# Performance work log

Hardware: AMD Instinct MI355X
Metric: run time of the kernel (lower is better)

Reference implementation:

```python
import jax, jax.numpy as jnp
import numpy as np

N = 100000   # num_nodes
D = 128      # input_dim
DO = 128     # output_dim
V = 3        # num_views/relations
E = 500000   # edges per view
C = 2        # num_classes
H = D // 2   # label-attention hidden
VH = DO // 2 # view-attention hidden
EPS = 1e-5


def setup_inputs() -> dict:
    key = jax.random.key(0)
    ks = jax.random.split(key, 20)
    s = 0.05
    def nrm(k, shape):
        return jax.random.normal(k, shape, dtype=jnp.float32) * s
    return {
        'features': jax.random.normal(ks[0], (N, D), dtype=jnp.float32),
        'edge_src': jax.random.randint(ks[1], (V, E), 0, N, dtype=jnp.int32),
        'edge_dst': jax.random.randint(ks[2], (V, E), 0, N, dtype=jnp.int32),
        'edge_w': jax.random.uniform(ks[3], (V, E), dtype=jnp.float32),
        'clsW': nrm(ks[4], (D, C)), 'clsb': jnp.zeros((C,), jnp.float32),
        'attW1': nrm(ks[5], (C, D, H)), 'attb1': jnp.zeros((C, H), jnp.float32),
        'attW2': nrm(ks[6], (C, H)), 'attb2': jnp.zeros((C,), jnp.float32),
        'att_bias': jnp.float32(0.1),
        'relW': nrm(ks[7], (V, D, DO)), 'relb': jnp.zeros((V, DO), jnp.float32),
        'gateW': nrm(ks[8], (V, DO, DO)), 'gateb': jnp.zeros((V, DO), jnp.float32),
        'view_pref': jax.random.normal(ks[9], (V, DO), dtype=jnp.float32),
        'vattW1': nrm(ks[10], (DO, VH)), 'vattb1': jnp.zeros((VH,), jnp.float32),
        'vattW2': nrm(ks[11], (VH,)), 'vattb2': jnp.float32(0.0),
        'selfW': nrm(ks[12], (D, DO)), 'selfb': jnp.zeros((DO,), jnp.float32),
        'featW': nrm(ks[13], (D, DO)), 'featb': jnp.zeros((DO,), jnp.float32),
        'fusW': nrm(ks[14], (2 * DO, DO)), 'fusb': jnp.zeros((DO,), jnp.float32),
        'ln_g': jnp.ones((DO,), jnp.float32), 'ln_b': jnp.zeros((DO,), jnp.float32),
    }


def reference(features, edge_src, edge_dst, edge_w,
              clsW, clsb, attW1, attb1, attW2, attb2, att_bias,
              relW, relb, gateW, gateb,
              view_pref, vattW1, vattb1, vattW2, vattb2,
              selfW, selfb, featW, featb, fusW, fusb, ln_g, ln_b):
    # --- LabelAwareAttention ---
    class_probs = jax.nn.softmax(features @ clsW + clsb, axis=-1)          # [N,C]
    h = jax.nn.relu(jnp.einsum('nd,cdh->cnh', features, attW1) + attb1[:, None, :])
    scores = jax.nn.sigmoid(jnp.einsum('cnh,ch->cn', h, attW2) + attb2[:, None])
    node_att = jnp.sum(scores.T * class_probs, axis=-1) + att_bias         # [N]

    # --- per-view RelationAggregator (num_relations=1 -> relation weight is 1) ---
    src_f = features[edge_src]                                             # [V,E,D]
    msg = (jnp.einsum('ved,vdo->veo', src_f, relW) + relb[:, None, :]) \
          * edge_w[..., None]                                              # [V,E,DO]
    agg = jax.vmap(lambda m, d: jax.ops.segment_sum(m, d, num_segments=N))(
        msg, edge_dst)                                                     # [V,N,DO]
    gate = jax.nn.sigmoid(jnp.einsum('vno,vop->vnp', agg, gateW) + gateb[:, None, :])
    view_out = gate * agg                                                  # [V,N,DO]

    # --- ViewLevelAttention ---
    vh = jax.nn.relu(jnp.einsum('vno,oh->vnh', view_out * view_pref[:, None, :], vattW1) + vattb1)
    vscores = jnp.einsum('vnh,h->vn', vh, vattW2) + vattb2                 # [V,N]
    vweights = jax.nn.softmax(vscores, axis=0)                             # softmax over views
    combined = jnp.sum(view_out * vweights[..., None], axis=0)             # [N,DO]

    # --- fusion + residual + layer norm (dropout=0, eval) ---
    self_out = features @ selfW + selfb
    transformed = features @ featW + featb
    weighted = combined * node_att[:, None]
    fused = jax.nn.relu(jnp.concatenate([self_out, weighted], axis=-1) @ fusW + fusb)
    out = fused + transformed
    mu = jnp.mean(out, axis=-1, keepdims=True)
    var = jnp.var(out, axis=-1, keepdims=True)
    out = (out - mu) / jnp.sqrt(var + EPS) * ln_g + ln_b
    return out, class_probs
```

## Files before the change

### kernel.cpp

```cpp
#include <hip/hip_runtime.h>
#include <hip/hip_bf16.h>

#define NN 100000
#define DD 128
#define VV 3
#define EE 500000
#define TOT (VV * NN)
#define NB ((TOT + 255) / 256)
#define RGB ((NN + 127) / 128)

typedef unsigned short u16;
typedef unsigned int u32;
typedef short s8v __attribute__((ext_vector_type(8)));
typedef float f4v __attribute__((ext_vector_type(4)));

__device__ __forceinline__ float bf2f(u16 u) {
    return __uint_as_float(((u32)u) << 16);
}
__device__ __forceinline__ u16 f2bf(float f) {
    u32 x = __float_as_uint(f);
    u32 r = (x + 0x7fffu + ((x >> 16) & 1u)) >> 16;
    return (u16)r;
}

// ... 86 lines not shown
    #pragma unroll
    for (int rep = 0; rep < 512 / NT; ++rep) {
        int flat = rep * NT + tid;
        int n = flat >> 4;
        int c8 = flat & 15;
        uint4 q = *reinterpret_cast<const uint4*>(src + (size_t)n * 128 + c8 * 8);
        float* d = Xs + n * XSTR + c8 * 8;
        d[0] = bf2f((u16)(q.x & 0xffffu)); d[1] = bf2f((u16)(q.x >> 16));
        d[2] = bf2f((u16)(q.y & 0xffffu)); d[3] = bf2f((u16)(q.y >> 16));
        d[4] = bf2f((u16)(q.z & 0xffffu)); d[5] = bf2f((u16)(q.z >> 16));
        d[6] = bf2f((u16)(q.w & 0xffffu)); d[7] = bf2f((u16)(q.w >> 16));
    }
}


__device__ __forceinline__ void stageWf(u16 (*Wf)[136], const u16* __restrict__ src, int tid) {
    #pragma unroll
    for (int rep = 0; rep < 8; ++rep) {
        int flat = rep * 256 + tid;
        int n = flat >> 4, c8 = flat & 15;
        *reinterpret_cast<uint4*>(&Wf[n][c8 * 8]) =
            *reinterpret_cast<const uint4*>(src + (size_t)n * DD + c8 * 8);
    }
}

__device__ __forceinline__ void stageWtHalf(u16 (*Wt)[72], const u16* __restrict__ src, int tid) {
    #pragma unroll
    for (int rep = 0; rep < 4; ++rep) {
        int flat = rep * 256 + tid;
        int n = flat >> 3, c8 = flat & 7;
        *reinterpret_cast<uint4*>(&Wt[n][c8 * 8]) =
            *reinterpret_cast<const uint4*>(src + (size_t)n * DD + c8 * 8);
    }
}

__device__ __forceinline__ void stageX(u16 (*Wf)[136], const u16* __restrict__ src,
                                       int row0, int tid) {
    #pragma unroll
    for (int rep = 0; rep < 8; ++rep) {
        int flat = rep * 256 + tid;
        int n = flat >> 4, c8 = flat & 15;
        int gr = row0 + n; if (gr >= NN) gr = NN - 1;
        *reinterpret_cast<uint4*>(&Wf[n][c8 * 8]) =
            *reinterpret_cast<const uint4*>(src + (size_t)gr * DD + c8 * 8);
    }
}

__device__ __forceinline__ void loadFrags(s8v af[2][2][2], u16 (*Wf)[136],
                                          int wv, int l15, int quad) {
    #pragma unroll
    for (int h = 0; h < 2; ++h)
        #pragma unroll
        for (int t = 0; t < 2; ++t) {
            int kl = h * 64 + t * 32 + quad * 8;
            af[h][t][0] = *reinterpret_cast<const s8v*>(&Wf[wv * 32 + l15][kl]);
            af[h][t][1] = *reinterpret_cast<const s8v*>(&Wf[wv * 32 + 16 + l15][kl]);
        }
}

__device__ __forceinline__ void mfmaWt8(f4v acc[2][8], const s8v af[2][2][2], int h,
                                        u16 (*Wt)[72], int l15, int quad) {
    #pragma unroll
    for (int t = 0; t < 2; ++t) {
        int kl = t * 32 + quad * 8;
        #pragma unroll
        for (int c = 0; c < 8; ++c) {
            s8v b = *reinterpret_cast<const s8v*>(&Wt[c * 16 + l15][kl]);
            acc[0][c] = __builtin_amdgcn_mfma_f32_16x16x32_bf16(af[h][t][0], b, acc[0][c], 0, 0, 0);
            acc[1][c] = __builtin_amdgcn_mfma_f32_16x16x32_bf16(af[h][t][1], b, acc[1][c], 0, 0, 0);
        }
    }
}

__device__ __forceinline__ void mfmaWfFull(f4v acc[2][8], const s8v af[2][2][2],
                                           u16 (*Wf)[136], int l15, int quad) {
    #pragma unroll
    for (int h = 0; h < 2; ++h)
        #pragma unroll
        for (int t = 0; t < 2; ++t) {
            int kl = h * 64 + t * 32 + quad * 8;
            #pragma unroll
            for (int c = 0; c < 8; ++c) {
                s8v b = *reinterpret_cast<const s8v*>(&Wf[c * 16 + l15][kl]);
                acc[0][c] = __builtin_amdgcn_mfma_f32_16x16x32_bf16(af[h][t][0], b, acc[0][c], 0, 0, 0);
                acc[1][c] = __builtin_amdgcn_mfma_f32_16x16x32_bf16(af[h][t][1], b, acc[1][c], 0, 0, 0);
            }
        }
}

__global__ void prep_kernel(const float* __restrict__ selfW, const float* __restrict__ selfb,
                            const float* __restrict__ fusW, const float* __restrict__ fusb,
                            float* __restrict__ Wsf, float* __restrict__ c1) {
    int o = threadIdx.x;
    int k = blockIdx.x;
    if (k < 128) {
        float acc = 0.f;
        for (int m = 0; m < 128; ++m)
            acc += selfW[k * 128 + m] * fusW[m * 128 + o];
// ... 206 lines not shown
    int src = 0, dst = 0; float w = 0.f;
    if (lane == 0) {
        src = esrc[eg]; dst = edst[eg]; w = ew[eg];
    }
    src = __shfl(src, 0, 32);
    dst = __shfl(dst, 0, 32);
    w   = __shfl(w, 0, 32);
    const float* fr = feat + (size_t)src * DD + lane * 4;
    float4 q = *reinterpret_cast<const float4*>(fr);
    u16* outp = aggB + ((size_t)v * NN + dst) * DD + lane * 4;
    atomAddBf16x2(outp,     w * q.x, w * q.y);
    atomAddBf16x2(outp + 2, w * q.z, w * q.w);
    if (lane == 0) atomicAdd(wsum + v * NN + dst, w);
}

__global__ __launch_bounds__(256) void fused_mfma_kernel(
        const u16* __restrict__ featB, const u16* __restrict__ aggB,
        const u16* __restrict__ attW1B,
        const float* __restrict__ clsW, const float* __restrict__ clsb,
        const float* __restrict__ attb1, const float* __restrict__ attW2,
        const float* __restrict__ attb2, const float* __restrict__ att_bias,
        const u16* __restrict__ relWb, const float* __restrict__ relb,
        const u16* __restrict__ W12b, const float* __restrict__ rgbv,
        const float* __restrict__ gateb,
        const u16* __restrict__ vattW1p, const float* __restrict__ vattb1,
        const float* __restrict__ vattW2, const float* __restrict__ vattb2,
        const float* __restrict__ wsum,
        const u16* __restrict__ WsfB, const u16* __restrict__ featWB,
        const u16* __restrict__ fusWbB,
        const float* __restrict__ c1, const float* __restrict__ featb,
        const float* __restrict__ ln_g, const float* __restrict__ ln_b,
        float* __restrict__ outp, float* __restrict__ probs_out) {
    __shared__ u16 Wf[128][136];
    __shared__ u16 Wt[128][72];
    int tid = threadIdx.x;
    int wv = tid >> 6, lane = tid & 63;
    int quad = lane >> 4, l15 = lane & 15;
    int row0 = blockIdx.x * 128;
    const float L2E = 1.4426950408889634f;

    float na[2][4];
    {
        stageX(Wf, featB, row0, tid);
        stageWtHalf(Wt, attW1B, tid);
        __syncthreads();
        s8v af[2][2][2];
        loadFrags(af, Wf, wv, l15, quad);
        f4v accL[2][8];
        #pragma unroll
        for (int rt = 0; rt < 2; ++rt)
            #pragma unroll
            for (int c = 0; c < 8; ++c)
                accL[rt][c] = f4v{0.f, 0.f, 0.f, 0.f};
        mfmaWt8(accL, af, 0, Wt, l15, quad);
        __syncthreads();
        stageWtHalf(Wt, attW1B + 64, tid);
        __syncthreads();
        mfmaWt8(accL, af, 1, Wt, l15, quad);

        float ab1[8], aw2[8];
        #pragma unroll
        for (int c = 0; c < 8; ++c) {
            int col = c * 16 + l15;
            ab1[c] = attb1[col];
            aw2[c] = attW2[col];
        }
        float cw0[8], cw1[8];
        #pragma unroll
        for (int j = 0; j < 8; ++j) {
            int k = l15 * 8 + j;
            cw0[j] = clsW[k * 2];
            cw1[j] = clsW[k * 2 + 1];
        }
        float cb0 = clsb[0], cb1 = clsb[1];
        float b20 = attb2[0], b21 = attb2[1];
        float abias = att_bias[0];

        #pragma unroll
        for (int rt = 0; rt < 2; ++rt)
            #pragma unroll
            for (int r = 0; r < 4; ++r) {
                int n = wv * 32 + rt * 16 + quad * 4 + r;
                int gr = row0 + n;
                float p0 = 0.f, p1 = 0.f;
                #pragma unroll
                for (int c = 0; c < 4; ++c) {
                    float hv = accL[rt][c][r] + ab1[c];
                    hv = hv > 0.f ? hv : 0.f;
                    p0 += hv * aw2[c];
                }
                #pragma unroll
                for (int c = 4; c < 8; ++c) {
                    float hv = accL[rt][c][r] + ab1[c];
                    hv = hv > 0.f ? hv : 0.f;
                    p1 += hv * aw2[c];
                }
                uint4 q = *reinterpret_cast<const uint4*>(&Wf[n][l15 * 8]);
                float f[8];
                f[0] = bf2f((u16)(q.x & 0xffffu)); f[1] = bf2f((u16)(q.x >> 16));
                f[2] = bf2f((u16)(q.y & 0xffffu)); f[3] = bf2f((u16)(q.y >> 16));
                f[4] = bf2f((u16)(q.z & 0xffffu)); f[5] = bf2f((u16)(q.z >> 16));
                f[6] = bf2f((u16)(q.w & 0xffffu)); f[7] = bf2f((u16)(q.w >> 16));
                float l0 = 0.f, l1 = 0.f;
                #pragma unroll
                for (int j = 0; j < 8; ++j) {
                    l0 = fmaf(f[j], cw0[j], l0);
                    l1 = fmaf(f[j], cw1[j], l1);
                }
                #pragma unroll
                for (int m = 1; m < 16; m <<= 1) {
                    p0 += __shfl_xor(p0, m);
                    p1 += __shfl_xor(p1, m);
                    l0 += __shfl_xor(l0, m);
                    l1 += __shfl_xor(l1, m);
                }
                float s0 = 1.f / (1.f + expf(-(p0 + b20)));
                float s1 = 1.f / (1.f + expf(-(p1 + b21)));
                l0 += cb0; l1 += cb1;
                float mm = fmaxf(l0, l1);
                float e0 = expf(l0 - mm), e1 = expf(l1 - mm);
                float inv = 1.f / (e0 + e1);
                float q0 = e0 * inv, q1 = e1 * inv;
                na[rt][r] = q0 * s0 + q1 * s1 + abias;
                if (l15 == 0 && gr < NN) {
                    probs_out[gr * 2]     = q0;
                    probs_out[gr * 2 + 1] = q1;
                }
            }
    }

    float Cacc[2][8][4];
    float mrun[2][4], Srun[2][4];
    #pragma unroll
    for (int rt = 0; rt < 2; ++rt)
        #pragma unroll
        for (int r = 0; r < 4; ++r) { mrun[rt][r] = -3.0e38f; Srun[rt][r] = 0.f; }
    #pragma unroll
    for (int rt = 0; rt < 2; ++rt)
        #pragma unroll
        for (int c = 0; c < 8; ++c)
            #pragma unroll
            for (int r = 0; r < 4; ++r) Cacc[rt][c][r] = 0.f;

    for (int v = 0; v < VV; ++v) {
        const size_t vbase = (size_t)v * NN;
        __syncthreads();
        stageX(Wf, aggB + vbase * DD, row0, tid);
        __syncthreads();
        s8v af[2][2][2];
        loadFrags(af, Wf, wv, l15, quad);
        __syncthreads();
        const u16* W1 = relWb + (size_t)v * DD * DD;
        const u16* W2 = W12b + (size_t)v * DD * DD;
        stageWf(Wf, W1, tid);
        stageWtHalf(Wt, W2, tid);
        __syncthreads();
        f4v acc2[2][8];
        #pragma unroll
        for (int rt = 0; rt < 2; ++rt)
            #pragma unroll
            for (int c = 0; c < 8; ++c)
                acc2[rt][c] = f4v{0.f, 0.f, 0.f, 0.f};
        mfmaWt8(acc2, af, 0, Wt, l15, quad);
        __syncthreads();
        stageWtHalf(Wt, W2 + 64, tid);
        __syncthreads();
        mfmaWt8(acc2, af, 1, Wt, l15, quad);

        float wsn[2][4];
        #pragma unroll
        for (int rt = 0; rt < 2; ++rt)
            #pragma unroll
            for (int r = 0; r < 4; ++r) {
                int gr = row0 + wv * 32 + rt * 16 + quad * 4 + r;
                wsn[rt][r] = wsum[vbase + (gr < NN ? gr : NN - 1)];
            }
        u32 gpk[2][8][2];
        #pragma unroll
        for (int c = 0; c < 8; ++c) {
            int col = c * 16 + l15;
            float rg2 = rgbv[v * DD + col];
            float gb2 = gateb[v * DD + col];
            #pragma unroll
            for (int rt = 0; rt < 2; ++rt)
                #pragma unroll
                for (int rp = 0; rp < 2; ++rp) {
                    float g0 = fsigmoid(acc2[rt][c][2 * rp]     + wsn[rt][2 * rp] * rg2 + gb2);
                    float g1 = fsigmoid(acc2[rt][c][2 * rp + 1] + wsn[rt][2 * rp + 1] * rg2 + gb2);
                    gpk[rt][c][rp] = (u32)f2bf(g0) | ((u32)f2bf(g1) << 16);
                }
        }
        f4v acc1[2][8];
        #pragma unroll
        for (int rt = 0; rt < 2; ++rt)
            #pragma unroll
            for (int c = 0; c < 8; ++c)
                acc1[rt][c] = f4v{0.f, 0.f, 0.f, 0.f};
        mfmaWfFull(acc1, af, Wf, l15, quad);
        #pragma unroll
        for (int c = 0; c < 8; ++c) {
            float rbc = relb[v * DD + c * 16 + l15];
            #pragma unroll
            for (int rt = 0; rt < 2; ++rt)
                #pragma unroll
                for (int r = 0; r < 4; ++r) {
                    float a = acc1[rt][c][r] + wsn[rt][r] * rbc;
                    u32 gp = gpk[rt][c][r >> 1];
                    float g = bf2f((u16)((r & 1) ? (gp >> 16) : (gp & 0xffffu)));
                    acc1[rt][c][r] = g * a;
                }
        }
        __syncthreads();
        #pragma unroll
        for (int rt = 0; rt < 2; ++rt)
            #pragma unroll
            for (int c = 0; c < 8; ++c)
                #pragma unroll
                for (int r = 0; r < 4; ++r)
                    Wf[wv * 32 + rt * 16 + quad * 4 + r][c * 16 + l15] =
                        f2bf(acc1[rt][c][r]);
        {
            const u16* Wv = vattW1p + (size_t)v * 64 * DD;
            #pragma unroll
            for (int rep = 0; rep < 4; ++rep) {
                int flat = rep * 256 + tid;
                int n = flat >> 4, c8 = flat & 15;
                uint4 q = *reinterpret_cast<const uint4*>(Wv + (size_t)n * DD + c8 * 8);
                int half = c8 >> 3;
                *reinterpret_cast<uint4*>(&Wt[half * 64 + n][(c8 & 7) * 8]) = q;
            }
        }
        __syncthreads();
        s8v a2[2][2][2];
        loadFrags(a2, Wf, wv, l15, quad);
        f4v acc3[2][4];
        #pragma unroll
        for (int rt = 0; rt < 2; ++rt)
            #pragma unroll
            for (int c = 0; c < 4; ++c)
                acc3[rt][c] = f4v{0.f, 0.f, 0.f, 0.f};
        #pragma unroll
        for (int h = 0; h < 2; ++h)
            #pragma unroll
            for (int t = 0; t < 2; ++t) {
                int kl = t * 32 + quad * 8;
                #pragma unroll
                for (int c = 0; c < 4; ++c) {
                    s8v b = *reinterpret_cast<const s8v*>(&Wt[h * 64 + c * 16 + l15][kl]);
                    acc3[0][c] = __builtin_amdgcn_mfma_f32_16x16x32_bf16(a2[h][t][0], b, acc3[0][c], 0, 0, 0);
                    acc3[1][c] = __builtin_amdgcn_mfma_f32_16x16x32_bf16(a2[h][t][1], b, acc3[1][c], 0, 0, 0);
                }
            }
        float vb1[4], vw2[4];
        #pragma unroll
        for (int c = 0; c < 4; ++c) {
            int col = c * 16 + l15;
            vb1[c] = vattb1[col];
            vw2[c] = vattW2[col];
        }
        float vb2 = vattb2[0];
        #pragma unroll
        for (int rt = 0; rt < 2; ++rt)
            #pragma unroll
            for (int r = 0; r < 4; ++r) {
                float p = 0.f;
                #pragma unroll
                for (int c = 0; c < 4; ++c) {
                    float hv = acc3[rt][c][r] + vb1[c];
                    hv = hv > 0.f ? hv : 0.f;
                    p += hv * vw2[c];
                }
                #pragma unroll
                for (int m = 1; m < 16; m <<= 1)
                    p += __shfl_xor(p, m);
                float s = p + vb2;
                float mn = fmaxf(mrun[rt][r], s);
                float sc = fexp2((mrun[rt][r] - mn) * L2E);
                float es = fexp2((s - mn) * L2E);
                Srun[rt][r] = Srun[rt][r] * sc + es;
                mrun[rt][r] = mn;
                #pragma unroll
                for (int c = 0; c < 8; ++c)
                    Cacc[rt][c][r] = Cacc[rt][c][r] * sc + es * acc1[rt][c][r];
            }
    }

    float wrow[2][4];
    #pragma unroll
    for (int rt = 0; rt < 2; ++rt)
        #pragma unroll
        for (int r = 0; r < 4; ++r)
            wrow[rt][r] = na[rt][r] * frcp(Srun[rt][r]);
    __syncthreads();
    #pragma unroll
    for (int rt = 0; rt < 2; ++rt)
        #pragma unroll
        for (int c = 0; c < 8; ++c)
            #pragma unroll
            for (int r = 0; r < 4; ++r)
                Wf[wv * 32 + rt * 16 + quad * 4 + r][c * 16 + l15] =
                    f2bf(Cacc[rt][c][r] * wrow[rt][r]);
    __syncthreads();
    s8v a2[2][2][2];
    loadFrags(a2, Wf, wv, l15, quad);
    __syncthreads();
    stageX(Wf, featB, row0, tid);
    __syncthreads();
    s8v af[2][2][2];
    loadFrags(af, Wf, wv, l15, quad);
    __syncthreads();
    stageWf(Wf, WsfB, tid);
    stageWtHalf(Wt, featWB, tid);
    __syncthreads();
    f4v acc1[2][8], acc2[2][8];
    #pragma unroll
    for (int rt = 0; rt < 2; ++rt)
        #pragma unroll
        for (int c = 0; c < 8; ++c) {
            acc1[rt][c] = f4v{0.f, 0.f, 0.f, 0.f};
            acc2[rt][c] = f4v{0.f, 0.f, 0.f, 0.f};
        }
    mfmaWfFull(acc1, af, Wf, l15, quad);
    mfmaWt8(acc2, af, 0, Wt, l15, quad);
    __syncthreads();
    stageWf(Wf, fusWbB, tid);
    stageWtHalf(Wt, featWB + 64, tid);
    __syncthreads();
    mfmaWt8(acc2, af, 1, Wt, l15, quad);
    mfmaWfFull(acc1, a2, Wf, l15, quad);

    float c1j[8], fbj[8], gj[8], bj[8];
    #pragma unroll
    for (int c = 0; c < 8; ++c) {
        int col = c * 16 + l15;
        c1j[c] = c1[col];
        fbj[c] = featb[col];
        gj[c]  = ln_g[col];
        bj[c]  = ln_b[col];
    }
    #pragma unroll
    for (int rt = 0; rt < 2; ++rt)
        #pragma unroll
        for (int c = 0; c < 8; ++c)
            #pragma unroll
            for (int r = 0; r < 4; ++r) {
                float f = acc1[rt][c][r] + c1j[c];
                f = f > 0.f ? f : 0.f;
                acc1[rt][c][r] = f + acc2[rt][c][r] + fbj[c];
            }
    #pragma unroll
    for (int rt = 0; rt < 2; ++rt)
        #pragma unroll
        for (int r = 0; r < 4; ++r) {
            float s = 0.f, q = 0.f;
            #pragma unroll
            for (int c = 0; c < 8; ++c) {
                float x = acc1[rt][c][r];
                s += x; q += x * x;
            }
            #pragma unroll
            for (int m = 1; m < 16; m <<= 1) {
                s += __shfl_xor(s, m);
                q += __shfl_xor(q, m);
            }
            float mu = s * (1.f / 128.f);
            float var = q * (1.f / 128.f) - mu * mu;
            float rs = rsqrtf(var + 1e-5f);
            int gr = row0 + wv * 32 + rt * 16 + quad * 4 + r;
            if (gr < NN) {
                #pragma unroll
                for (int c = 0; c < 8; ++c)
                    outp[(size_t)gr * DD + c * 16 + l15] =
                        (acc1[rt][c][r] - mu) * rs * gj[c] + bj[c];
            }
        }
}

__global__ __launch_bounds__(256) void label_kernel(
        const float* __restrict__ feat, const float* __restrict__ clsW, const float* __restrict__ clsb,
        const float* __restrict__ attW1, const float* __restrict__ attb1,
        const float* __restrict__ attW2, const float* __restrict__ attb2,
        const float* __restrict__ att_bias,
        float* __restrict__ node_att, float* __restrict__ probs_out) {
    __shared__ float Xs[32][132];
    __shared__ float Ws[64][132];
    int tid = threadIdx.x;
    int row0 = blockIdx.x * 32;
    stage_x_f32<132, 256>(&Xs[0][0], feat + (size_t)row0 * DD, tid);
// ... 59 lines not shown
    }
    __syncthreads();
    if (tid < 32) {
        int n = tid;
        float l0 = Lsc[n * 2], l1 = Lsc[n * 2 + 1];
        float m = fmaxf(l0, l1);
        float e0 = expf(l0 - m), e1 = expf(l1 - m);
        float inv = 1.f / (e0 + e1);
        float p0 = e0 * inv, p1 = e1 * inv;
        float na = p0 * Ssc[n * 2] + p1 * Ssc[n * 2 + 1] + att_bias[0];
        int row = row0 + n;
        node_att[row] = na;
        probs_out[row * 2]     = p0;
        probs_out[row * 2 + 1] = p1;
    }
}

__global__ __launch_bounds__(256) void relgate_kernel(
        const float* __restrict__ relW, const float* __restrict__ relb,
        const float* __restrict__ gateW, const float* __restrict__ gateb,
        u16* __restrict__ aggB, const float* __restrict__ wsum) {
    __shared__ float Xs[32][128];
    __shared__ float Ws[64][132];
    int tid = threadIdx.x;
    int v = blockIdx.y;
    int row0 = blockIdx.x * 32;
    u16* base = aggB + ((size_t)v * NN + row0) * DD;
    stage_x_bf16<128, 256>(&Xs[0][0], base, tid);
    int to = tid & 31, tn = tid >> 5;
    int o0 = to * 4, n0 = tn * 4;
// ... 118 lines not shown
    float m = fmaxf(s0, fmaxf(s1, s2));
    float e0 = expf(s0 - m), e1 = expf(s1 - m), e2 = expf(s2 - m);
    float inv = 1.f / (e0 + e1 + e2);
    float w0 = e0 * inv, w1 = e1 * inv, w2 = e2 * inv;
    float na = node_att[n];
    size_t off = (size_t)n * DD + c4 * 4;
    ushort4 q0 = *reinterpret_cast<const ushort4*>(aggB + off);
    ushort4 q1 = *reinterpret_cast<const ushort4*>(aggB + (size_t)NN * DD + off);
    ushort4 q2 = *reinterpret_cast<const ushort4*>(aggB + 2 * (size_t)NN * DD + off);
    ushort4 r;
    r.x = f2bf((bf2f(q0.x) * w0 + bf2f(q1.x) * w1 + bf2f(q2.x) * w2) * na);
    r.y = f2bf((bf2f(q0.y) * w0 + bf2f(q1.y) * w1 + bf2f(q2.y) * w2) * na);
    r.z = f2bf((bf2f(q0.z) * w0 + bf2f(q1.z) * w1 + bf2f(q2.z) * w2) * na);
    r.w = f2bf((bf2f(q0.w) * w0 + bf2f(q1.w) * w1 + bf2f(q2.w) * w2) * na);
    *reinterpret_cast<ushort4*>(aggB + off) = r;
}

__global__ __launch_bounds__(256) void final_kernel(
        const float* __restrict__ feat, const u16* __restrict__ weightedB,
        const float* __restrict__ Wsf, const float* __restrict__ c1,
        const float* __restrict__ fusW, const float* __restrict__ featW,
        const float* __restrict__ featb, const float* __restrict__ ln_g,
        const float* __restrict__ ln_b, float* __restrict__ outp) {
    __shared__ float Xs[32][128];
    __shared__ float Ws[64][128];
    int tid = threadIdx.x;
    int row0 = blockIdx.x * 32;
    stage_x_f32<128, 256>(&Xs[0][0], feat + (size_t)row0 * DD, tid);
    int to = tid & 31, tn = tid >> 5;
    int o0 = to * 4, n0 = tn * 4;
// ... 123 lines not shown
    int2*  bsw  = (int2*)(bs + NB + 1);
    u16* featB  = (u16*)(bsw + (size_t)VV * EE);
    size_t needed = (size_t)((char*)(featB + (size_t)NN * DD) - (char*)d_ws);

    float* outp  = (float*)d_out;
    float* probs = outp + (size_t)NN * DD;

    prep_kernel<<<129, 128, 0, stream>>>(selfW, selfb, fusW, fusb, Wsf, c1);
    if (ws_size >= needed) {
        featconv_kernel<<<12500, 256, 0, stream>>>(feat, featB);
        wprep_kernel<<<384, 128, 0, stream>>>(relW, gateW, relWb, gateWb);
        wprep2_kernel<<<128, 128, 0, stream>>>(Wsf, featW, fusW, WsfB, featWB, fusWbB);
        wprep3_kernel<<<128, 128, 0, stream>>>(attW1, attW1B);
        wprep4_kernel<<<192, 128, 0, stream>>>(vattW1, view_pref, vattW1p);
        wprep5_kernel<<<VV * 129, 128, 0, stream>>>(relW, gateW, relb, W12b, rgb);
        hipMemsetAsync(C, 0, (size_t)TOT * sizeof(int), stream);
        count_kernel<<<(VV * EE + 255) / 256, 256, 0, stream>>>(edst, C);
        scanA_kernel<<<NB, 256, 0, stream>>>(C, bs);
        scanB_kernel<<<1, 1024, 0, stream>>>(bs);
        scanC_kernel<<<NB, 256, 0, stream>>>(C, bs);
        fill_kernel<<<(VV * EE + 255) / 256, 256, 0, stream>>>(esrc, edst, ew, C, bsw);
        gather_kernel<<<(VV * NN) / 4, 256, 0, stream>>>(featB, C, bsw, aggB, wsum);
        fused_mfma_kernel<<<RGB, 256, 0, stream>>>(
            featB, aggB, attW1B, clsW, clsb, attb1, attW2, attb2, att_bias,
            relWb, relb, W12b, rgb, gateb,
            vattW1p, vattb1, vattW2, vattb2, wsum,
            WsfB, featWB, fusWbB, c1, featb, ln_g, ln_b, outp, probs);
    } else {
        label_kernel<<<3125, 256, 0, stream>>>(feat, clsW, clsb, attW1, attb1, attW2, attb2,
                                               att_bias, natt, probs);
        hipMemsetAsync(d_ws, 0,
                       (size_t)VV * NN * DD * sizeof(u16) + (size_t)VV * NN * sizeof(float),
                       stream);
        scatter_kernel<<<187500, 256, 0, stream>>>(esrc, edst, ew, feat, aggB, wsum);
        relgate_kernel<<<dim3(3125, 3), 256, 0, stream>>>(relW, relb, gateW, gateb, aggB, wsum);
        vatt_kernel<<<dim3(3125, 3), 128, 0, stream>>>(aggB, view_pref, vattW1, vattb1,
                                                       vattW2, vattb2, vsc);
        combine_kernel<<<12500, 256, 0, stream>>>(aggB, vsc, natt);
        final_kernel<<<3125, 256, 0, stream>>>(feat, aggB, Wsf, c1, fusW, featW, featb,
                                               ln_g, ln_b, outp);
    }
}
// ... 1 lines not shown
```

Before: 715.4 us.

## Split fused MFMA kernel into label, per-view relgate, and final kernels

The single fused per-row-block kernel is split into three MFMA kernels. The label attention runs separately, the relation and gate step runs as a per-view grid that writes view_out back to aggB along with view scores, and a final kernel does the view softmax, combine, fusion and layer norm. Weight B-fragments are now read straight from global memory instead of being staged in shared memory. The goal is more parallelism (three times the blocks in the relgate stage) and lower shared-memory and register pressure, at the cost of an extra round trip of view_out through global memory and more kernel launches.

```diff
diff --git a/kernel.cpp b/kernel.cpp
--- a/kernel.cpp
+++ b/kernel.cpp
@@ -124,36 +124,20 @@
 }
 
 
-__device__ __forceinline__ void stageWf(u16 (*Wf)[136], const u16* __restrict__ src, int tid) {
-    #pragma unroll
-    for (int rep = 0; rep < 8; ++rep) {
-        int flat = rep * 256 + tid;
-        int n = flat >> 4, c8 = flat & 15;
-        *reinterpret_cast<uint4*>(&Wf[n][c8 * 8]) =
-            *reinterpret_cast<const uint4*>(src + (size_t)n * DD + c8 * 8);
-    }
-}
-
-__device__ __forceinline__ void stageWtHalf(u16 (*Wt)[72], const u16* __restrict__ src, int tid) {
-    #pragma unroll
-    for (int rep = 0; rep < 4; ++rep) {
-        int flat = rep * 256 + tid;
-        int n = flat >> 3, c8 = flat & 7;
-        *reinterpret_cast<uint4*>(&Wt[n][c8 * 8]) =
-            *reinterpret_cast<const uint4*>(src + (size_t)n * DD + c8 * 8);
-    }
-}
-
-__device__ __forceinline__ void stageX(u16 (*Wf)[136], const u16* __restrict__ src,
-                                       int row0, int tid) {
-    #pragma unroll
-    for (int rep = 0; rep < 8; ++rep) {
-        int flat = rep * 256 + tid;
-        int n = flat >> 4, c8 = flat & 15;
-        int gr = row0 + n; if (gr >= NN) gr = NN - 1;
-        *reinterpret_cast<uint4*>(&Wf[n][c8 * 8]) =
-            *reinterpret_cast<const uint4*>(src + (size_t)gr * DD + c8 * 8);
-    }
+__device__ __forceinline__ void loadFragsG(s8v af[2][2][2], const u16* __restrict__ X,
+                                           int row0, int wv, int l15, int quad) {
+    int r0 = row0 + wv * 32 + l15;
+    int r1 = r0 + 16;
+    if (r0 >= NN) r0 = NN - 1;
+    if (r1 >= NN) r1 = NN - 1;
+    #pragma unroll
+    for (int h = 0; h < 2; ++h)
+        #pragma unroll
+        for (int t = 0; t < 2; ++t) {
+            int kl = h * 64 + t * 32 + quad * 8;
+            af[h][t][0] = *reinterpret_cast<const s8v*>(X + (size_t)r0 * DD + kl);
+            af[h][t][1] = *reinterpret_cast<const s8v*>(X + (size_t)r1 * DD + kl);
+        }
 }
 
 __device__ __forceinline__ void loadFrags(s8v af[2][2][2], u16 (*Wf)[136],
@@ -168,22 +152,8 @@
         }
 }
 
-__device__ __forceinline__ void mfmaWt8(f4v acc[2][8], const s8v af[2][2][2], int h,
-                                        u16 (*Wt)[72], int l15, int quad) {
-    #pragma unroll
-    for (int t = 0; t < 2; ++t) {
-        int kl = t * 32 + quad * 8;
-        #pragma unroll
-        for (int c = 0; c < 8; ++c) {
-            s8v b = *reinterpret_cast<const s8v*>(&Wt[c * 16 + l15][kl]);
-            acc[0][c] = __builtin_amdgcn_mfma_f32_16x16x32_bf16(af[h][t][0], b, acc[0][c], 0, 0, 0);
-            acc[1][c] = __builtin_amdgcn_mfma_f32_16x16x32_bf16(af[h][t][1], b, acc[1][c], 0, 0, 0);
-        }
-    }
-}
-
-__device__ __forceinline__ void mfmaWfFull(f4v acc[2][8], const s8v af[2][2][2],
-                                           u16 (*Wf)[136], int l15, int quad) {
+__device__ __forceinline__ void mfmaG8(f4v acc[2][8], const s8v af[2][2][2],
+                                       const u16* __restrict__ W, int l15, int quad) {
     #pragma unroll
     for (int h = 0; h < 2; ++h)
         #pragma unroll
@@ -191,7 +161,7 @@
             int kl = h * 64 + t * 32 + quad * 8;
             #pragma unroll
             for (int c = 0; c < 8; ++c) {
-                s8v b = *reinterpret_cast<const s8v*>(&Wf[c * 16 + l15][kl]);
+                s8v b = *reinterpret_cast<const s8v*>(W + (size_t)(c * 16 + l15) * DD + kl);
                 acc[0][c] = __builtin_amdgcn_mfma_f32_16x16x32_bf16(af[h][t][0], b, acc[0][c], 0, 0, 0);
                 acc[1][c] = __builtin_amdgcn_mfma_f32_16x16x32_bf16(af[h][t][1], b, acc[1][c], 0, 0, 0);
             }
@@ -428,106 +398,86 @@
     if (lane == 0) atomicAdd(wsum + v * NN + dst, w);
 }
 
-__global__ __launch_bounds__(256) void fused_mfma_kernel(
-        const u16* __restrict__ featB, const u16* __restrict__ aggB,
-        const u16* __restrict__ attW1B,
+__global__ __launch_bounds__(256) void label_mfma_kernel(
+        const u16* __restrict__ featB, const u16* __restrict__ attW1B,
         const float* __restrict__ clsW, const float* __restrict__ clsb,
         const float* __restrict__ attb1, const float* __restrict__ attW2,
         const float* __restrict__ attb2, const float* __restrict__ att_bias,
-        const u16* __restrict__ relWb, const float* __restrict__ relb,
-        const u16* __restrict__ W12b, const float* __restrict__ rgbv,
-        const float* __restrict__ gateb,
-        const u16* __restrict__ vattW1p, const float* __restrict__ vattb1,
-        const float* __restrict__ vattW2, const float* __restrict__ vattb2,
-        const float* __restrict__ wsum,
-        const u16* __restrict__ WsfB, const u16* __restrict__ featWB,
-        const u16* __restrict__ fusWbB,
-        const float* __restrict__ c1, const float* __restrict__ featb,
-        const float* __restrict__ ln_g, const float* __restrict__ ln_b,
-        float* __restrict__ outp, float* __restrict__ probs_out) {
-    __shared__ u16 Wf[128][136];
-    __shared__ u16 Wt[128][72];
+        float* __restrict__ node_att, float* __restrict__ probs_out) {
     int tid = threadIdx.x;
     int wv = tid >> 6, lane = tid & 63;
     int quad = lane >> 4, l15 = lane & 15;
     int row0 = blockIdx.x * 128;
-    const float L2E = 1.4426950408889634f;
-
-    float na[2][4];
-    {
-        stageX(Wf, featB, row0, tid);
-        stageWtHalf(Wt, attW1B, tid);
-        __syncthreads();
-        s8v af[2][2][2];
-        loadFrags(af, Wf, wv, l15, quad);
-        f4v accL[2][8];
-        #pragma unroll
-        for (int rt = 0; rt < 2; ++rt)
-            #pragma unroll
-            for (int c = 0; c < 8; ++c)
-                accL[rt][c] = f4v{0.f, 0.f, 0.f, 0.f};
-        mfmaWt8(accL, af, 0, Wt, l15, quad);
-        __syncthreads();
-        stageWtHalf(Wt, attW1B + 64, tid);
-        __syncthreads();
-        mfmaWt8(accL, af, 1, Wt, l15, quad);
-
-        float ab1[8], aw2[8];
-        #pragma unroll
-        for (int c = 0; c < 8; ++c) {
-            int col = c * 16 + l15;
-            ab1[c] = attb1[col];
-            aw2[c] = attW2[col];
-        }
-        float cw0[8], cw1[8];
-        #pragma unroll
-        for (int j = 0; j < 8; ++j) {
-            int k = l15 * 8 + j;
-            cw0[j] = clsW[k * 2];
-            cw1[j] = clsW[k * 2 + 1];
-        }
-        float cb0 = clsb[0], cb1 = clsb[1];
-        float b20 = attb2[0], b21 = attb2[1];
-        float abias = att_bias[0];
-
-        #pragma unroll
-        for (int rt = 0; rt < 2; ++rt)
-            #pragma unroll
-            for (int r = 0; r < 4; ++r) {
-                int n = wv * 32 + rt * 16 + quad * 4 + r;
-                int gr = row0 + n;
-                float p0 = 0.f, p1 = 0.f;
-                #pragma unroll
-                for (int c = 0; c < 4; ++c) {
-                    float hv = accL[rt][c][r] + ab1[c];
-                    hv = hv > 0.f ? hv : 0.f;
-                    p0 += hv * aw2[c];
-                }
-                #pragma unroll
-                for (int c = 4; c < 8; ++c) {
-                    float hv = accL[rt][c][r] + ab1[c];
-                    hv = hv > 0.f ? hv : 0.f;
-                    p1 += hv * aw2[c];
-                }
-                uint4 q = *reinterpret_cast<const uint4*>(&Wf[n][l15 * 8]);
-                float f[8];
-                f[0] = bf2f((u16)(q.x & 0xffffu)); f[1] = bf2f((u16)(q.x >> 16));
-                f[2] = bf2f((u16)(q.y & 0xffffu)); f[3] = bf2f((u16)(q.y >> 16));
-                f[4] = bf2f((u16)(q.z & 0xffffu)); f[5] = bf2f((u16)(q.z >> 16));
-                f[6] = bf2f((u16)(q.w & 0xffffu)); f[7] = bf2f((u16)(q.w >> 16));
-                float l0 = 0.f, l1 = 0.f;
-                #pragma unroll
-                for (int j = 0; j < 8; ++j) {
-                    l0 = fmaf(f[j], cw0[j], l0);
-                    l1 = fmaf(f[j], cw1[j], l1);
-                }
-                #pragma unroll
-                for (int m = 1; m < 16; m <<= 1) {
-                    p0 += __shfl_xor(p0, m);
-                    p1 += __shfl_xor(p1, m);
-                    l0 += __shfl_xor(l0, m);
-                    l1 += __shfl_xor(l1, m);
-                }
+
+    s8v af[2][2][2];
+    loadFragsG(af, featB, row0, wv, l15, quad);
+
+    f4v acc[2][8];
+    #pragma unroll
+    for (int rt = 0; rt < 2; ++rt)
+        #pragma unroll
+        for (int c = 0; c < 8; ++c)
+            acc[rt][c] = f4v{0.f, 0.f, 0.f, 0.f};
+    mfmaG8(acc, af, attW1B, l15, quad);
+
+    float ab1[8], aw2[8];
+    #pragma unroll
+    for (int c = 0; c < 8; ++c) {
+        int col = c * 16 + l15;
+        ab1[c] = attb1[col];
+        aw2[c] = attW2[col];
+    }
+    float cw0[8], cw1[8];
+    #pragma unroll
+    for (int j = 0; j < 8; ++j) {
+        int k = l15 * 8 + j;
+        cw0[j] = clsW[k * 2];
+        cw1[j] = clsW[k * 2 + 1];
+    }
+    float cb0 = clsb[0], cb1 = clsb[1];
+    float b20 = attb2[0], b21 = attb2[1];
+    float abias = att_bias[0];
+
+    #pragma unroll
+    for (int rt = 0; rt < 2; ++rt)
+        #pragma unroll
+        for (int r = 0; r < 4; ++r) {
+            int n = wv * 32 + rt * 16 + quad * 4 + r;
+            int gr = row0 + n;
+            int grc = gr < NN ? gr : NN - 1;
+            float p0 = 0.f, p1 = 0.f;
+            #pragma unroll
+            for (int c = 0; c < 4; ++c) {
+                float hv = acc[rt][c][r] + ab1[c];
+                hv = hv > 0.f ? hv : 0.f;
+                p0 += hv * aw2[c];
+            }
+            #pragma unroll
+            for (int c = 4; c < 8; ++c) {
+                float hv = acc[rt][c][r] + ab1[c];
+                hv = hv > 0.f ? hv : 0.f;
+                p1 += hv * aw2[c];
+            }
+            uint4 q = *reinterpret_cast<const uint4*>(featB + (size_t)grc * DD + l15 * 8);
+            float f[8];
+            f[0] = bf2f((u16)(q.x & 0xffffu)); f[1] = bf2f((u16)(q.x >> 16));
+            f[2] = bf2f((u16)(q.y & 0xffffu)); f[3] = bf2f((u16)(q.y >> 16));
+            f[4] = bf2f((u16)(q.z & 0xffffu)); f[5] = bf2f((u16)(q.z >> 16));
+            f[6] = bf2f((u16)(q.w & 0xffffu)); f[7] = bf2f((u16)(q.w >> 16));
+            float l0 = 0.f, l1 = 0.f;
+            #pragma unroll
+            for (int j = 0; j < 8; ++j) {
+                l0 = fmaf(f[j], cw0[j], l0);
+                l1 = fmaf(f[j], cw1[j], l1);
+            }
+            #pragma unroll
+            for (int m = 1; m < 16; m <<= 1) {
+                p0 += __shfl_xor(p0, m);
+                p1 += __shfl_xor(p1, m);
+                l0 += __shfl_xor(l0, m);
+                l1 += __shfl_xor(l1, m);
+            }
+            if (l15 == 0 && gr < NN) {
                 float s0 = 1.f / (1.f + expf(-(p0 + b20)));
                 float s1 = 1.f / (1.f + expf(-(p1 + b21)));
                 l0 += cb0; l1 += cb1;
@@ -535,257 +485,9 @@
                 float e0 = expf(l0 - mm), e1 = expf(l1 - mm);
                 float inv = 1.f / (e0 + e1);
                 float q0 = e0 * inv, q1 = e1 * inv;
-                na[rt][r] = q0 * s0 + q1 * s1 + abias;
-                if (l15 == 0 && gr < NN) {
-                    probs_out[gr * 2]     = q0;
-                    probs_out[gr * 2 + 1] = q1;
-                }
-            }
-    }
-
-    float Cacc[2][8][4];
-    float mrun[2][4], Srun[2][4];
-    #pragma unroll
-    for (int rt = 0; rt < 2; ++rt)
-        #pragma unroll
-        for (int r = 0; r < 4; ++r) { mrun[rt][r] = -3.0e38f; Srun[rt][r] = 0.f; }
-    #pragma unroll
-    for (int rt = 0; rt < 2; ++rt)
-        #pragma unroll
-        for (int c = 0; c < 8; ++c)
-            #pragma unroll
-            for (int r = 0; r < 4; ++r) Cacc[rt][c][r] = 0.f;
-
-    for (int v = 0; v < VV; ++v) {
-        const size_t vbase = (size_t)v * NN;
-        __syncthreads();
-        stageX(Wf, aggB + vbase * DD, row0, tid);
-        __syncthreads();
-        s8v af[2][2][2];
-        loadFrags(af, Wf, wv, l15, quad);
-        __syncthreads();
-        const u16* W1 = relWb + (size_t)v * DD * DD;
-        const u16* W2 = W12b + (size_t)v * DD * DD;
-        stageWf(Wf, W1, tid);
-        stageWtHalf(Wt, W2, tid);
-        __syncthreads();
-        f4v acc2[2][8];
-        #pragma unroll
-        for (int rt = 0; rt < 2; ++rt)
-            #pragma unroll
-            for (int c = 0; c < 8; ++c)
-                acc2[rt][c] = f4v{0.f, 0.f, 0.f, 0.f};
-        mfmaWt8(acc2, af, 0, Wt, l15, quad);
-        __syncthreads();
-        stageWtHalf(Wt, W2 + 64, tid);
-        __syncthreads();
-        mfmaWt8(acc2, af, 1, Wt, l15, quad);
-
-        float wsn[2][4];
-        #pragma unroll
-        for (int rt = 0; rt < 2; ++rt)
-            #pragma unroll
-            for (int r = 0; r < 4; ++r) {
-                int gr = row0 + wv * 32 + rt * 16 + quad * 4 + r;
-                wsn[rt][r] = wsum[vbase + (gr < NN ? gr : NN - 1)];
-            }
-        u32 gpk[2][8][2];
-        #pragma unroll
-        for (int c = 0; c < 8; ++c) {
-            int col = c * 16 + l15;
-            float rg2 = rgbv[v * DD + col];
-            float gb2 = gateb[v * DD + col];
-            #pragma unroll
-            for (int rt = 0; rt < 2; ++rt)
-                #pragma unroll
-                for (int rp = 0; rp < 2; ++rp) {
-                    float g0 = fsigmoid(acc2[rt][c][2 * rp]     + wsn[rt][2 * rp] * rg2 + gb2);
-                    float g1 = fsigmoid(acc2[rt][c][2 * rp + 1] + wsn[rt][2 * rp + 1] * rg2 + gb2);
-                    gpk[rt][c][rp] = (u32)f2bf(g0) | ((u32)f2bf(g1) << 16);
-                }
-        }
-        f4v acc1[2][8];
-        #pragma unroll
-        for (int rt = 0; rt < 2; ++rt)
-            #pragma unroll
-            for (int c = 0; c < 8; ++c)
-                acc1[rt][c] = f4v{0.f, 0.f, 0.f, 0.f};
-        mfmaWfFull(acc1, af, Wf, l15, quad);
-        #pragma unroll
-        for (int c = 0; c < 8; ++c) {
-            float rbc = relb[v * DD + c * 16 + l15];
-            #pragma unroll
-            for (int rt = 0; rt < 2; ++rt)
-                #pragma unroll
-                for (int r = 0; r < 4; ++r) {
-                    float a = acc1[rt][c][r] + wsn[rt][r] * rbc;
-                    u32 gp = gpk[rt][c][r >> 1];
-                    float g = bf2f((u16)((r & 1) ? (gp >> 16) : (gp & 0xffffu)));
-                    acc1[rt][c][r] = g * a;
-                }
-        }
-        __syncthreads();
-        #pragma unroll
-        for (int rt = 0; rt < 2; ++rt)
-            #pragma unroll
-            for (int c = 0; c < 8; ++c)
-                #pragma unroll
-                for (int r = 0; r < 4; ++r)
-                    Wf[wv * 32 + rt * 16 + quad * 4 + r][c * 16 + l15] =
-                        f2bf(acc1[rt][c][r]);
-        {
-            const u16* Wv = vattW1p + (size_t)v * 64 * DD;
-            #pragma unroll
-            for (int rep = 0; rep < 4; ++rep) {
-                int flat = rep * 256 + tid;
-                int n = flat >> 4, c8 = flat & 15;
-                uint4 q = *reinterpret_cast<const uint4*>(Wv + (size_t)n * DD + c8 * 8);
-                int half = c8 >> 3;
-                *reinterpret_cast<uint4*>(&Wt[half * 64 + n][(c8 & 7) * 8]) = q;
-            }
-        }
-        __syncthreads();
-        s8v a2[2][2][2];
-        loadFrags(a2, Wf, wv, l15, quad);
-        f4v acc3[2][4];
-        #pragma unroll
-        for (int rt = 0; rt < 2; ++rt)
-            #pragma unroll
-            for (int c = 0; c < 4; ++c)
-                acc3[rt][c] = f4v{0.f, 0.f, 0.f, 0.f};
-        #pragma unroll
-        for (int h = 0; h < 2; ++h)
-            #pragma unroll
-            for (int t = 0; t < 2; ++t) {
-                int kl = t * 32 + quad * 8;
-                #pragma unroll
-                for (int c = 0; c < 4; ++c) {
-                    s8v b = *reinterpret_cast<const s8v*>(&Wt[h * 64 + c * 16 + l15][kl]);
-                    acc3[0][c] = __builtin_amdgcn_mfma_f32_16x16x32_bf16(a2[h][t][0], b, acc3[0][c], 0, 0, 0);
-                    acc3[1][c] = __builtin_amdgcn_mfma_f32_16x16x32_bf16(a2[h][t][1], b, acc3[1][c], 0, 0, 0);
-                }
-            }
-        float vb1[4], vw2[4];
-        #pragma unroll
-        for (int c = 0; c < 4; ++c) {
-            int col = c * 16 + l15;
-            vb1[c] = vattb1[col];
-            vw2[c] = vattW2[col];
-        }
-        float vb2 = vattb2[0];
-        #pragma unroll
-        for (int rt = 0; rt < 2; ++rt)
-            #pragma unroll
-            for (int r = 0; r < 4; ++r) {
-                float p = 0.f;
-                #pragma unroll
-                for (int c = 0; c < 4; ++c) {
-                    float hv = acc3[rt][c][r] + vb1[c];
-                    hv = hv > 0.f ? hv : 0.f;
-                    p += hv * vw2[c];
-                }
-                #pragma unroll
-                for (int m = 1; m < 16; m <<= 1)
-                    p += __shfl_xor(p, m);
-                float s = p + vb2;
-                float mn = fmaxf(mrun[rt][r], s);
-                float sc = fexp2((mrun[rt][r] - mn) * L2E);
-                float es = fexp2((s - mn) * L2E);
-                Srun[rt][r] = Srun[rt][r] * sc + es;
-                mrun[rt][r] = mn;
-                #pragma unroll
-                for (int c = 0; c < 8; ++c)
-                    Cacc[rt][c][r] = Cacc[rt][c][r] * sc + es * acc1[rt][c][r];
-            }
-    }
-
-    float wrow[2][4];
-    #pragma unroll
-    for (int rt = 0; rt < 2; ++rt)
-        #pragma unroll
-        for (int r = 0; r < 4; ++r)
-            wrow[rt][r] = na[rt][r] * frcp(Srun[rt][r]);
-    __syncthreads();
-    #pragma unroll
-    for (int rt = 0; rt < 2; ++rt)
-        #pragma unroll
-        for (int c = 0; c < 8; ++c)
-            #pragma unroll
-            for (int r = 0; r < 4; ++r)
-                Wf[wv * 32 + rt * 16 + quad * 4 + r][c * 16 + l15] =
-                    f2bf(Cacc[rt][c][r] * wrow[rt][r]);
-    __syncthreads();
-    s8v a2[2][2][2];
-    loadFrags(a2, Wf, wv, l15, quad);
-    __syncthreads();
-    stageX(Wf, featB, row0, tid);
-    __syncthreads();
-    s8v af[2][2][2];
-    loadFrags(af, Wf, wv, l15, quad);
-    __syncthreads();
-    stageWf(Wf, WsfB, tid);
-    stageWtHalf(Wt, featWB, tid);
-    __syncthreads();
-    f4v acc1[2][8], acc2[2][8];
-    #pragma unroll
-    for (int rt = 0; rt < 2; ++rt)
-        #pragma unroll
-        for (int c = 0; c < 8; ++c) {
-            acc1[rt][c] = f4v{0.f, 0.f, 0.f, 0.f};
-            acc2[rt][c] = f4v{0.f, 0.f, 0.f, 0.f};
-        }
-    mfmaWfFull(acc1, af, Wf, l15, quad);
-    mfmaWt8(acc2, af, 0, Wt, l15, quad);
-    __syncthreads();
-    stageWf(Wf, fusWbB, tid);
-    stageWtHalf(Wt, featWB + 64, tid);
-    __syncthreads();
-    mfmaWt8(acc2, af, 1, Wt, l15, quad);
-    mfmaWfFull(acc1, a2, Wf, l15, quad);
-
-    float c1j[8], fbj[8], gj[8], bj[8];
-    #pragma unroll
-    for (int c = 0; c < 8; ++c) {
-        int col = c * 16 + l15;
-        c1j[c] = c1[col];
-        fbj[c] = featb[col];
-        gj[c]  = ln_g[col];
-        bj[c]  = ln_b[col];
-    }
-    #pragma unroll
-    for (int rt = 0; rt < 2; ++rt)
-        #pragma unroll
-        for (int c = 0; c < 8; ++c)
-            #pragma unroll
-            for (int r = 0; r < 4; ++r) {
-                float f = acc1[rt][c][r] + c1j[c];
-                f = f > 0.f ? f : 0.f;
-                acc1[rt][c][r] = f + acc2[rt][c][r] + fbj[c];
-            }
-    #pragma unroll
-    for (int rt = 0; rt < 2; ++rt)
-        #pragma unroll
-        for (int r = 0; r < 4; ++r) {
-            float s = 0.f, q = 0.f;
-            #pragma unroll
-            for (int c = 0; c < 8; ++c) {
-                float x = acc1[rt][c][r];
-                s += x; q += x * x;
-            }
-            #pragma unroll
-            for (int m = 1; m < 16; m <<= 1) {
-                s += __shfl_xor(s, m);
-                q += __shfl_xor(q, m);
-            }
-            float mu = s * (1.f / 128.f);
-            float var = q * (1.f / 128.f) - mu * mu;
-            float rs = rsqrtf(var + 1e-5f);
-            int gr = row0 + wv * 32 + rt * 16 + quad * 4 + r;
-            if (gr < NN) {
-                #pragma unroll
-                for (int c = 0; c < 8; ++c)
-                    outp[(size_t)gr * DD + c * 16 + l15] =
-                        (acc1[rt][c][r] - mu) * rs * gj[c] + bj[c];
+                node_att[gr] = q0 * s0 + q1 * s1 + abias;
+                probs_out[gr * 2]     = q0;
+                probs_out[gr * 2 + 1] = q1;
             }
         }
 }
@@ -875,6 +577,142 @@
         probs_out[row * 2]     = p0;
         probs_out[row * 2 + 1] = p1;
     }
+}
+
+__global__ __launch_bounds__(256, 3) void relgate_mfma_kernel(
+        const u16* __restrict__ relWb, const float* __restrict__ relb,
+        const u16* __restrict__ W12b, const float* __restrict__ rgbv,
+        const float* __restrict__ gateb,
+        const u16* __restrict__ vattW1p, const float* __restrict__ vattb1,
+        const float* __restrict__ vattW2, const float* __restrict__ vattb2,
+        u16* __restrict__ aggB, const float* __restrict__ wsum,
+        float* __restrict__ vscores) {
+    __shared__ u16 Wf[128][136];
+    int tid = threadIdx.x;
+    int wv = tid >> 6, lane = tid & 63;
+    int quad = lane >> 4, l15 = lane & 15;
+    int v = blockIdx.y;
+    int row0 = blockIdx.x * 128;
+    const size_t vbase = (size_t)v * NN;
+
+    s8v af[2][2][2];
+    loadFragsG(af, aggB + vbase * DD, row0, wv, l15, quad);
+
+    const u16* W1 = relWb + (size_t)v * DD * DD;
+    const u16* W2 = W12b + (size_t)v * DD * DD;
+
+    float wsn[2][4];
+    #pragma unroll
+    for (int rt = 0; rt < 2; ++rt)
+        #pragma unroll
+        for (int r = 0; r < 4; ++r) {
+            int gr = row0 + wv * 32 + rt * 16 + quad * 4 + r;
+            wsn[rt][r] = wsum[vbase + (gr < NN ? gr : NN - 1)];
+        }
+
+    f4v acc2[2][8];
+    #pragma unroll
+    for (int rt = 0; rt < 2; ++rt)
+        #pragma unroll
+        for (int c = 0; c < 8; ++c)
+            acc2[rt][c] = f4v{0.f, 0.f, 0.f, 0.f};
+    mfmaG8(acc2, af, W2, l15, quad);
+
+    u32 gpk[2][8][2];
+    #pragma unroll
+    for (int c = 0; c < 8; ++c) {
+        int col = c * 16 + l15;
+        float rg2 = rgbv[v * DD + col];
+        float gb2 = gateb[v * DD + col];
+        #pragma unroll
+        for (int rt = 0; rt < 2; ++rt)
+            #pragma unroll
+            for (int rp = 0; rp < 2; ++rp) {
+                float g0 = fsigmoid(acc2[rt][c][2 * rp]     + wsn[rt][2 * rp] * rg2 + gb2);
+                float g1 = fsigmoid(acc2[rt][c][2 * rp + 1] + wsn[rt][2 * rp + 1] * rg2 + gb2);
+                gpk[rt][c][rp] = (u32)f2bf(g0) | ((u32)f2bf(g1) << 16);
+            }
+    }
+
+    f4v acc1[2][8];
+    #pragma unroll
+    for (int rt = 0; rt < 2; ++rt)
+        #pragma unroll
+        for (int c = 0; c < 8; ++c)
+            acc1[rt][c] = f4v{0.f, 0.f, 0.f, 0.f};
+    mfmaG8(acc1, af, W1, l15, quad);
+
+    #pragma unroll
+    for (int c = 0; c < 8; ++c) {
+        float rbc = relb[v * DD + c * 16 + l15];
+        #pragma unroll
+        for (int rt = 0; rt < 2; ++rt)
+            #pragma unroll
+            for (int r = 0; r < 4; ++r) {
+                float a = acc1[rt][c][r] + wsn[rt][r] * rbc;
+                u32 gp = gpk[rt][c][r >> 1];
+                float g = bf2f((u16)((r & 1) ? (gp >> 16) : (gp & 0xffffu)));
+                Wf[wv * 32 + rt * 16 + quad * 4 + r][c * 16 + l15] = f2bf(g * a);
+            }
+    }
+
+    #pragma unroll
+    for (int rep = 0; rep < 8; ++rep) {
+        int n = wv * 32 + rep * 4 + quad;
+        int gr = row0 + n;
+        if (gr < NN)
+            *reinterpret_cast<uint4*>(aggB + (vbase + gr) * DD + l15 * 8) =
+                *reinterpret_cast<const uint4*>(&Wf[n][l15 * 8]);
+    }
+
+    s8v a2[2][2][2];
+    loadFrags(a2, Wf, wv, l15, quad);
+    const u16* Wv = vattW1p + (size_t)v * 64 * DD;
+    f4v acc3[2][4];
+    #pragma unroll
+    for (int rt = 0; rt < 2; ++rt)
+        #pragma unroll
+        for (int c = 0; c < 4; ++c)
+            acc3[rt][c] = f4v{0.f, 0.f, 0.f, 0.f};
+    #pragma unroll
+    for (int h = 0; h < 2; ++h)
+        #pragma unroll
+        for (int t = 0; t < 2; ++t) {
+            int kl = t * 32 + quad * 8;
+            #pragma unroll
+            for (int c = 0; c < 4; ++c) {
+                s8v b = *reinterpret_cast<const s8v*>(
+                    Wv + (size_t)(c * 16 + l15) * DD + h * 64 + kl);
+                acc3[0][c] = __builtin_amdgcn_mfma_f32_16x16x32_bf16(a2[h][t][0], b, acc3[0][c], 0, 0, 0);
+                acc3[1][c] = __builtin_amdgcn_mfma_f32_16x16x32_bf16(a2[h][t][1], b, acc3[1][c], 0, 0, 0);
+            }
+        }
+    float vb1[4], vw2[4];
+    #pragma unroll
+    for (int c = 0; c < 4; ++c) {
+        int col = c * 16 + l15;
+        vb1[c] = vattb1[col];
+        vw2[c] = vattW2[col];
+    }
+    float vb2 = vattb2[0];
+    #pragma unroll
+    for (int rt = 0; rt < 2; ++rt)
+        #pragma unroll
+        for (int r = 0; r < 4; ++r) {
+            float p = 0.f;
+            #pragma unroll
+            for (int c = 0; c < 4; ++c) {
+                float hv = acc3[rt][c][r] + vb1[c];
+                hv = hv > 0.f ? hv : 0.f;
+                p += hv * vw2[c];
+            }
+            #pragma unroll
+            for (int m = 1; m < 16; m <<= 1)
+                p += __shfl_xor(p, m);
+            int gr = row0 + wv * 32 + rt * 16 + quad * 4 + r;
+            if (l15 == 0 && gr < NN)
+                vscores[vbase + gr] = p + vb2;
+        }
 }
 
 __global__ __launch_bounds__(256) void relgate_kernel(
@@ -1023,6 +861,124 @@
     r.z = f2bf((bf2f(q0.z) * w0 + bf2f(q1.z) * w1 + bf2f(q2.z) * w2) * na);
     r.w = f2bf((bf2f(q0.w) * w0 + bf2f(q1.w) * w1 + bf2f(q2.w) * w2) * na);
     *reinterpret_cast<ushort4*>(aggB + off) = r;
+}
+
+__global__ __launch_bounds__(256, 3) void final_mfma_kernel(
+        const u16* __restrict__ featB, const u16* __restrict__ aggB,
+        const float* __restrict__ vsc, const float* __restrict__ natt,
+        const u16* __restrict__ WsfB, const u16* __restrict__ featWB,
+        const u16* __restrict__ fusWbB,
+        const float* __restrict__ c1, const float* __restrict__ featb,
+        const float* __restrict__ ln_g, const float* __restrict__ ln_b,
+        float* __restrict__ outp) {
+    __shared__ u16 Wf[128][136];
+    __shared__ float rw[3][128];
+    int tid = threadIdx.x;
+    int wv = tid >> 6, lane = tid & 63;
+    int quad = lane >> 4, l15 = lane & 15;
+    int row0 = blockIdx.x * 128;
+
+    if (tid < 128) {
+        int gr = row0 + tid; if (gr >= NN) gr = NN - 1;
+        float s0 = vsc[gr], s1 = vsc[NN + gr], s2 = vsc[2 * NN + gr];
+        float m = fmaxf(s0, fmaxf(s1, s2));
+        const float L2E = 1.4426950408889634f;
+        float e0 = fexp2((s0 - m) * L2E);
+        float e1 = fexp2((s1 - m) * L2E);
+        float e2 = fexp2((s2 - m) * L2E);
+        float na = natt[gr] * frcp(e0 + e1 + e2);
+        rw[0][tid] = e0 * na;
+        rw[1][tid] = e1 * na;
+        rw[2][tid] = e2 * na;
+    }
+
+    s8v af[2][2][2];
+    loadFragsG(af, featB, row0, wv, l15, quad);
+
+    f4v acc1[2][8], acc2[2][8];
+    #pragma unroll
+    for (int rt = 0; rt < 2; ++rt)
+        #pragma unroll
+        for (int c = 0; c < 8; ++c) {
+            acc1[rt][c] = f4v{0.f, 0.f, 0.f, 0.f};
+            acc2[rt][c] = f4v{0.f, 0.f, 0.f, 0.f};
+        }
+    mfmaG8(acc1, af, WsfB, l15, quad);
+    mfmaG8(acc2, af, featWB, l15, quad);
+    __syncthreads();
+
+    #pragma unroll
+    for (int rep = 0; rep < 8; ++rep) {
+        int n = wv * 32 + rep * 4 + quad;
+        int gr = row0 + n; if (gr >= NN) gr = NN - 1;
+        size_t off = (size_t)gr * DD + l15 * 8;
+        uint4 q0 = *reinterpret_cast<const uint4*>(aggB + off);
+        uint4 q1 = *reinterpret_cast<const uint4*>(aggB + (size_t)NN * DD + off);
+        uint4 q2 = *reinterpret_cast<const uint4*>(aggB + 2 * (size_t)NN * DD + off);
+        float w0 = rw[0][n], w1 = rw[1][n], w2 = rw[2][n];
+        u32 o[4];
+        const u32* a = &q0.x; const u32* b = &q1.x; const u32* c = &q2.x;
+        #pragma unroll
+        for (int j = 0; j < 4; ++j) {
+            float lo = bf2f((u16)(a[j] & 0xffffu)) * w0 + bf2f((u16)(b[j] & 0xffffu)) * w1
+                     + bf2f((u16)(c[j] & 0xffffu)) * w2;
+            float hi = bf2f((u16)(a[j] >> 16)) * w0 + bf2f((u16)(b[j] >> 16)) * w1
+                     + bf2f((u16)(c[j] >> 16)) * w2;
+            o[j] = (u32)f2bf(lo) | ((u32)f2bf(hi) << 16);
+        }
+        uint4 r; r.x = o[0]; r.y = o[1]; r.z = o[2]; r.w = o[3];
+        *reinterpret_cast<uint4*>(&Wf[n][l15 * 8]) = r;
+    }
+
+    s8v a2[2][2][2];
+    loadFrags(a2, Wf, wv, l15, quad);
+    mfmaG8(acc1, a2, fusWbB, l15, quad);
+
+    float c1j[8], fbj[8], gj[8], bj[8];
+    #pragma unroll
+    for (int c = 0; c < 8; ++c) {
+        int col = c * 16 + l15;
+        c1j[c] = c1[col];
+        fbj[c] = featb[col];
+        gj[c]  = ln_g[col];
+        bj[c]  = ln_b[col];
+    }
+    #pragma unroll
+    for (int rt = 0; rt < 2; ++rt)
+        #pragma unroll
+        for (int c = 0; c < 8; ++c)
+            #pragma unroll
+            for (int r = 0; r < 4; ++r) {
+                float f = acc1[rt][c][r] + c1j[c];
+                f = f > 0.f ? f : 0.f;
+                acc1[rt][c][r] = f + acc2[rt][c][r] + fbj[c];
+            }
+    #pragma unroll
+    for (int rt = 0; rt < 2; ++rt)
+        #pragma unroll
+        for (int r = 0; r < 4; ++r) {
+            float s = 0.f, q = 0.f;
+            #pragma unroll
+            for (int c = 0; c < 8; ++c) {
+                float x = acc1[rt][c][r];
+                s += x; q += x * x;
+            }
+            #pragma unroll
+            for (int m = 1; m < 16; m <<= 1) {
+                s += __shfl_xor(s, m);
+                q += __shfl_xor(q, m);
+            }
+            float mu = s * (1.f / 128.f);
+            float var = q * (1.f / 128.f) - mu * mu;
+            float rs = rsqrtf(var + 1e-5f);
+            int gr = row0 + wv * 32 + rt * 16 + quad * 4 + r;
+            if (gr < NN) {
+                #pragma unroll
+                for (int c = 0; c < 8; ++c)
+                    outp[(size_t)gr * DD + c * 16 + l15] =
+                        (acc1[rt][c][r] - mu) * rs * gj[c] + bj[c];
+            }
+        }
 }
 
 __global__ __launch_bounds__(256) void final_kernel(
@@ -1176,6 +1132,8 @@
         wprep3_kernel<<<128, 128, 0, stream>>>(attW1, attW1B);
         wprep4_kernel<<<192, 128, 0, stream>>>(vattW1, view_pref, vattW1p);
         wprep5_kernel<<<VV * 129, 128, 0, stream>>>(relW, gateW, relb, W12b, rgb);
+        label_mfma_kernel<<<RGB, 256, 0, stream>>>(featB, attW1B, clsW, clsb, attb1,
+                                                   attW2, attb2, att_bias, natt, probs);
         hipMemsetAsync(C, 0, (size_t)TOT * sizeof(int), stream);
         count_kernel<<<(VV * EE + 255) / 256, 256, 0, stream>>>(edst, C);
         scanA_kernel<<<NB, 256, 0, stream>>>(C, bs);
@@ -1183,11 +1141,12 @@
         scanC_kernel<<<NB, 256, 0, stream>>>(C, bs);
         fill_kernel<<<(VV * EE + 255) / 256, 256, 0, stream>>>(esrc, edst, ew, C, bsw);
         gather_kernel<<<(VV * NN) / 4, 256, 0, stream>>>(featB, C, bsw, aggB, wsum);
-        fused_mfma_kernel<<<RGB, 256, 0, stream>>>(
-            featB, aggB, attW1B, clsW, clsb, attb1, attW2, attb2, att_bias,
-            relWb, relb, W12b, rgb, gateb,
-            vattW1p, vattb1, vattW2, vattb2, wsum,
-            WsfB, featWB, fusWbB, c1, featb, ln_g, ln_b, outp, probs);
+        relgate_mfma_kernel<<<dim3(RGB, 3), 256, 0, stream>>>(relWb, relb, W12b, rgb, gateb,
+                                                              vattW1p, vattb1, vattW2, vattb2,
+                                                              aggB, wsum, vsc);
+        final_mfma_kernel<<<RGB, 256, 0, stream>>>(featB, aggB, vsc, natt,
+                                                   WsfB, featWB, fusWbB,
+                                                   c1, featb, ln_g, ln_b, outp);
     } else {
         label_kernel<<<3125, 256, 0, stream>>>(feat, clsW, clsb, attW1, attb1, attW2, attb2,
                                                att_bias, natt, probs);
```

Measured after the change: 755.9 us. 1.06x slower.
